# Optimization experiments

Measured on AMD Instinct MI355X. Metric: run time of the kernel, lower is better.

## Reference

```python
import jax, jax.numpy as jnp
import numpy as np

N_NODES = 100000
N_EDGES = 1600000
NUM_GRAPHS = 128
EPS = 1e-5


def setup_inputs() -> dict:
    key = jax.random.key(0)
    ks = jax.random.split(key, 8)
    x = jax.random.normal(ks[0], (N_NODES, 8), dtype=jnp.float32)
    edge_index = jax.random.randint(ks[1], (2, N_EDGES), 0, N_NODES, dtype=jnp.int64)
    batch = jnp.sort(jax.random.randint(ks[2], (N_NODES,), 0, NUM_GRAPHS, dtype=jnp.int64))
    W1_l = jax.random.normal(ks[3], (128, 8), dtype=jnp.float32) * 0.3
    b1 = jnp.zeros((128,), dtype=jnp.float32)
    W1_r = jax.random.normal(ks[4], (128, 8), dtype=jnp.float32) * 0.3
    g1 = jnp.ones((128,), dtype=jnp.float32)
    beta1 = jnp.zeros((128,), dtype=jnp.float32)
    W2_l = jax.random.normal(ks[5], (128, 128), dtype=jnp.float32) * 0.08
    b2 = jnp.zeros((128,), dtype=jnp.float32)
    W2_r = jax.random.normal(ks[6], (128, 128), dtype=jnp.float32) * 0.08
    g2 = jnp.ones((128,), dtype=jnp.float32)
    beta2 = jnp.zeros((128,), dtype=jnp.float32)
    return dict(x=x, edge_index=edge_index, batch=batch,
                W1_l=W1_l, b1=b1, W1_r=W1_r, g1=g1, beta1=beta1,
                W2_l=W2_l, b2=b2, W2_r=W2_r, g2=g2, beta2=beta2)


def _sage_conv(x, src, dst, W_l, b, W_r):
    # PyG SAGEConv: out = lin_l(mean_j x_j) + lin_r(x_i); lin_r has no bias
    msg = x[src]                                              # [E, F]
    agg = jax.ops.segment_sum(msg, dst, num_segments=N_NODES)
    deg = jax.ops.segment_sum(jnp.ones((src.shape[0],), x.dtype), dst,
                              num_segments=N_NODES)
    agg = agg / jnp.maximum(deg, 1.0)[:, None]                # mean aggregation
    return agg @ W_l.T + b + x @ W_r.T


def _batch_norm(h, gamma, beta):
    # training-mode BN over the node dimension
    mu = jnp.mean(h, axis=0)
    var = jnp.mean(jnp.square(h - mu), axis=0)
    return gamma * (h - mu) * jax.lax.rsqrt(var + EPS) + beta


def reference(x, edge_index, batch, W1_l, b1, W1_r, g1, beta1,
              W2_l, b2, W2_r, g2, beta2):
    src, dst = edge_index[0], edge_index[1]
    x1 = jax.nn.relu(_batch_norm(_sage_conv(x, src, dst, W1_l, b1, W1_r), g1, beta1))
    x2 = jax.nn.relu(_batch_norm(_sage_conv(x1, src, dst, W2_l, b2, W2_r), g2, beta2))
    h = x1 + x2  # dropout is identity in eval mode
    # global mean pool per graph
    s = jax.ops.segment_sum(h, batch, num_segments=NUM_GRAPHS)
    cnt = jax.ops.segment_sum(jnp.ones((h.shape[0],), h.dtype), batch,
                              num_segments=NUM_GRAPHS)
    return s / jnp.maximum(cnt, 1.0)[:, None]                 # [NUM_GRAPHS, 128]
```

## Files before the change

### kernel.cpp

```cpp
#include <hip/hip_runtime.h>
#include <cstdint>
#include <cstddef>

namespace {

constexpr int N_NODES = 100000;
constexpr int N_EDGES = 1600000;
constexpr int NUM_GRAPHS = 128;
constexpr int F = 128;
constexpr float BN_EPS = 1e-5f;

constexpr int W_BUCK = 512;
constexpr int NBUCK = (N_NODES + W_BUCK - 1) / W_BUCK;
constexpr int CB = 400;
constexpr int CHUNK = N_EDGES / CB;

typedef float f32x4 __attribute__((ext_vector_type(4)));
typedef float f32x2 __attribute__((ext_vector_type(2)));
typedef short s16x8 __attribute__((ext_vector_type(8)));
typedef unsigned char uchar;
union B8 { uint4 u; s16x8 s; };

__device__ inline ushort f2bf(float x) {
    uint u = __float_as_uint(x);
    u += 0x7fffu + ((u >> 16) & 1u);
    return (ushort)(u >> 16);
}
__device__ inline float bf2f(ushort s) { return __uint_as_float(((uint)s) << 16); }
__device__ inline uint pack2(float lo, float hi) {
    return (uint)f2bf(lo) | ((uint)f2bf(hi) << 16);
}
__device__ inline float bflo(uint u) { return __uint_as_float(u << 16); }
__device__ inline float bfhi(uint u) { return __uint_as_float(u & 0xffff0000u); }

__device__ inline void acc4f8(float* a, uint u) {
    f32x2 lo = __builtin_amdgcn_cvt_pk_f32_fp8((int)u, false);
    f32x2 hi = __builtin_amdgcn_cvt_pk_f32_fp8((int)u, true);
    a[0] += lo[0]; a[1] += lo[1]; a[2] += hi[0]; a[3] += hi[1];
}


__global__ void __launch_bounds__(256) k_histA(const int* __restrict__ ei,
                                               int* __restrict__ gcount) {
    __shared__ int bins[NBUCK];
    int t = threadIdx.x;
    for (int i = t; i < NBUCK; i += 256) bins[i] = 0;
    __syncthreads();
    int e0 = blockIdx.x * CHUNK;
    for (int i = t; i < CHUNK; i += 256)
        atomicAdd(&bins[ei[N_EDGES + e0 + i] >> 9], 1);
    __syncthreads();
    for (int i = t; i < NBUCK; i += 256) gcount[i * CB + blockIdx.x] = bins[i];
}

__global__ void __launch_bounds__(512) k_scanA(int* __restrict__ g,
                                               int* __restrict__ bsum) {
    __shared__ int tmp[512];
    int b = blockIdx.x, t = threadIdx.x;
    int v = (t < CB) ? g[b * CB + t] : 0;
    tmp[t] = v;
    __syncthreads();
    #pragma unroll
    for (int d = 1; d < 512; d <<= 1) {
        int u = (t >= d) ? tmp[t - d] : 0;
        __syncthreads();
        tmp[t] += u;
        __syncthreads();
    }
    if (t < CB) g[b * CB + t] = tmp[t] - v;
    if (t == 511) bsum[b] = tmp[511];
}

__global__ void __launch_bounds__(256) k_scanB(int* __restrict__ bsum) {
    __shared__ int tmp[256];
    int t = threadIdx.x;
    int v = (t < NBUCK) ? bsum[t] : 0;
    tmp[t] = v;
    __syncthreads();
    #pragma unroll
    for (int d = 1; d < 256; d <<= 1) {
        int u = (t >= d) ? tmp[t - d] : 0;
        __syncthreads();
        tmp[t] += u;
        __syncthreads();
    }
    if (t < NBUCK) bsum[t] = tmp[t] - v;
}

__global__ void __launch_bounds__(256) k_part(const int* __restrict__ ei,
                                              const int* __restrict__ gloc,
                                              const int* __restrict__ bsum,
                                              uint* __restrict__ epk) {
    __shared__ int cur[NBUCK];
    int t = threadIdx.x;
    for (int i = t; i < NBUCK; i += 256)
        cur[i] = gloc[i * CB + blockIdx.x] + bsum[i];
    __syncthreads();
    int e0 = blockIdx.x * CHUNK;
    for (int i = t; i < CHUNK; i += 256) {
        int d = ei[N_EDGES + e0 + i];
        int s = ei[e0 + i];
        int p = atomicAdd(&cur[d >> 9], 1);
        epk[p] = ((uint)s << 9) | (uint)(d & 511);
    }
}

__global__ void __launch_bounds__(512) k_rank(const uint* __restrict__ epk,
                                              const int* __restrict__ bsum,
                                              int* __restrict__ offs,
                                              int* __restrict__ ssrc) {
    __shared__ int dcnt[W_BUCK];
    __shared__ int tmp[W_BUCK];
    __shared__ int cur[W_BUCK];
    int b = blockIdx.x, t = threadIdx.x;
    dcnt[t] = 0;
    __syncthreads();
    int s0 = bsum[b];
    int s1 = (b + 1 < NBUCK) ? bsum[b + 1] : N_EDGES;
    for (int i = s0 + t; i < s1; i += 512)
        atomicAdd(&dcnt[epk[i] & 511u], 1);
    __syncthreads();
    int v = dcnt[t];
    tmp[t] = v;
    __syncthreads();
    #pragma unroll
    for (int d = 1; d < 512; d <<= 1) {
        int u = (t >= d) ? tmp[t - d] : 0;
        __syncthreads();
        tmp[t] += u;
        __syncthreads();
    }
    int start = s0 + tmp[t] - v;
    int node = b * W_BUCK + t;
    if (node <= N_NODES) offs[node] = start;
    cur[t] = start;
    __syncthreads();
    for (int i = s0 + t; i < s1; i += 512) {
        uint u = epk[i];
        int p = atomicAdd(&cur[u & 511u], 1);
        ssrc[p] = (int)(u >> 9);
    }
}


__global__ void k_bound(const int* __restrict__ batch, int* __restrict__ gstart) {
    int i = blockIdx.x * 256 + threadIdx.x;
    if (i >= N_NODES) return;
    int b = batch[i];
    if (i == 0) {
        for (int g = 0; g <= b; ++g) gstart[g] = 0;
    } else {
        int p = batch[i - 1];
        if (p != b) for (int g = p + 1; g <= b; ++g) gstart[g] = i;
    }
    if (i == N_NODES - 1) {
        for (int g = b + 1; g <= NUM_GRAPHS; ++g) gstart[g] = N_NODES;
    }
}


__global__ void k_packbf(const float* __restrict__ Wl, const float* __restrict__ Wr,
                         ushort* __restrict__ Wcat) {
    int i = blockIdx.x * 256 + threadIdx.x;
    int f = i >> 7, k = i & 127;
    Wcat[f * 256 + k]       = f2bf(Wl[i]);
    Wcat[f * 256 + 128 + k] = f2bf(Wr[i]);
}

__global__ void k_packbf1(const float* __restrict__ W1l, const float* __restrict__ W1r,
                          ushort* __restrict__ Wcat1) {
    int i = blockIdx.x * 256 + threadIdx.x;
    int f = i >> 5, k = i & 31;
    float v = (k < 8) ? W1r[f * 8 + k] : ((k < 16) ? W1l[f * 8 + (k - 8)] : 0.f);
    Wcat1[i] = f2bf(v);
}


__global__ void k_agg1(const float* __restrict__ x, const int* __restrict__ offs,
                       const int* __restrict__ ssrc, ushort* __restrict__ xa) {
    int n = blockIdx.x * 256 + threadIdx.x;
    if (n >= N_NODES) return;
    int s0 = offs[n], s1 = offs[n + 1];
    float a0=0,a1=0,a2=0,a3=0,a4=0,a5=0,a6=0,a7=0;
    int j = s0;
    for (; j + 3 < s1; j += 4) {
        int sa = ssrc[j], sb = ssrc[j+1], sc = ssrc[j+2], sd = ssrc[j+3];
        const float4* pa = (const float4*)(x + (size_t)sa * 8);
        const float4* pb = (const float4*)(x + (size_t)sb * 8);
        const float4* pc = (const float4*)(x + (size_t)sc * 8);
        const float4* pd = (const float4*)(x + (size_t)sd * 8);
        float4 va0 = pa[0], va1 = pa[1], vb0 = pb[0], vb1 = pb[1];
        float4 vc0 = pc[0], vc1 = pc[1], vd0 = pd[0], vd1 = pd[1];
        a0 += (va0.x + vb0.x) + (vc0.x + vd0.x);
        a1 += (va0.y + vb0.y) + (vc0.y + vd0.y);
        a2 += (va0.z + vb0.z) + (vc0.z + vd0.z);
        a3 += (va0.w + vb0.w) + (vc0.w + vd0.w);
        a4 += (va1.x + vb1.x) + (vc1.x + vd1.x);
        a5 += (va1.y + vb1.y) + (vc1.y + vd1.y);
        a6 += (va1.z + vb1.z) + (vc1.z + vd1.z);
        a7 += (va1.w + vb1.w) + (vc1.w + vd1.w);
    }
    for (; j < s1; ++j) {
        const float4* xp = (const float4*)(x + (size_t)ssrc[j] * 8);
        float4 b0 = xp[0], b1 = xp[1];
        a0+=b0.x; a1+=b0.y; a2+=b0.z; a3+=b0.w;
        a4+=b1.x; a5+=b1.y; a6+=b1.z; a7+=b1.w;
    }
    int dg = s1 - s0;
    float inv = 1.0f / (float)(dg > 1 ? dg : 1);
    const float4* xp = (const float4*)(x + (size_t)n * 8);
    float4 x0 = xp[0], x1v = xp[1];
    ushort* row = xa + (size_t)n * 32;
    uint4 o0 = {pack2(x0.x, x0.y), pack2(x0.z, x0.w), pack2(x1v.x, x1v.y), pack2(x1v.z, x1v.w)};
    uint4 o1 = {pack2(a0*inv, a1*inv), pack2(a2*inv, a3*inv),
                pack2(a4*inv, a5*inv), pack2(a6*inv, a7*inv)};
    uint4 z = {0u, 0u, 0u, 0u};
    *(uint4*)(row)      = o0;
    *(uint4*)(row + 8)  = o1;
    *(uint4*)(row + 16) = z;
    *(uint4*)(row + 24) = z;
}

__global__ void __launch_bounds__(256) k_lin1(
        const ushort* __restrict__ xa, const ushort* __restrict__ Wcat1,
        const float* __restrict__ b1, ushort* __restrict__ h1bf,
        float* __restrict__ stats) {
    __shared__ ushort sOut[64 * 140];
    __shared__ float sred[256];
    int tid = threadIdx.x;
    int wave = tid >> 6, lane = tid & 63;
    int quad = lane >> 4, l16 = lane & 15;
    int n0 = blockIdx.x * 64;

    int node = n0 + wave * 16 + l16;
    int cn = (node < N_NODES) ? node : N_NODES - 1;
    B8 ta;
    ta.u = *(const uint4*)(xa + (size_t)cn * 32 + quad * 8);

    #pragma unroll
    for (int nt = 0; nt < 8; ++nt) {
        int fb = nt * 16 + l16;
        B8 tb;
        tb.u = *(const uint4*)(Wcat1 + fb * 32 + quad * 8);
        f32x4 acc = {0.f, 0.f, 0.f, 0.f};
        acc = __builtin_amdgcn_mfma_f32_16x16x32_bf16(ta.s, tb.s, acc, 0, 0, 0);
        float bb = b1[fb];
        #pragma unroll
        for (int r = 0; r < 4; ++r) {
            int row = wave * 16 + quad * 4 + r;
            sOut[row * 140 + fb] = f2bf(acc[r] + bb);
        }
    }
    __syncthreads();

    #pragma unroll
    for (int p = 0; p < 4; ++p) {
        int row = p * 16 + (tid >> 4);
        int nd = n0 + row;
        if (nd < N_NODES) {
            int c0 = (tid & 15) * 8;
            uint4 v = *(const uint4*)&sOut[row * 140 + c0];
            *(uint4*)(h1bf + (size_t)nd * F + c0) = v;
        }
    }

    int f = tid & 127, half = tid >> 7;
    float s = 0.f, s2 = 0.f;
    for (int r = half * 32; r < half * 32 + 32; ++r) {
        if (n0 + r >= N_NODES) break;
        float v = bf2f(sOut[r * 140 + f]);
        s += v; s2 += v * v;
    }
    if (half) { sred[f] = s; sred[128 + f] = s2; }
    __syncthreads();
    if (!half) {
        s += sred[f]; s2 += sred[128 + f];
        atomicAdd(&stats[f], s);
        atomicAdd(&stats[F + f], s2);
    }
}

__global__ void k_bnfin(const float* __restrict__ stats, const float* __restrict__ gamma,
                        const float* __restrict__ beta, float* __restrict__ scsh) {
    int f = threadIdx.x;
    float mu  = stats[f] * (1.0f / N_NODES);
    float var = stats[F + f] * (1.0f / N_NODES) - mu * mu;
    float sc  = gamma[f] * rsqrtf(var + BN_EPS);
    scsh[f] = sc;
    scsh[F + f] = beta[f] - mu * sc;
}

__global__ void k_bnrelu(const ushort* __restrict__ h, const float* __restrict__ scsh,
                         ushort* __restrict__ x1bf, uchar* __restrict__ x1f8) {
    int i = blockIdx.x * 256 + threadIdx.x;
    int base = i * 8;
    int f = base & (F - 1);
    float4 sc0 = *(const float4*)(scsh + f);
    float4 sc1 = *(const float4*)(scsh + f + 4);
    float4 sh0 = *(const float4*)(scsh + F + f);
    float4 sh1 = *(const float4*)(scsh + F + f + 4);
    uint4 hv = *(const uint4*)(h + base);
    float v0 = fmaxf(0.f, bflo(hv.x)*sc0.x + sh0.x);
    float v1 = fmaxf(0.f, bfhi(hv.x)*sc0.y + sh0.y);
    float v2 = fmaxf(0.f, bflo(hv.y)*sc0.z + sh0.z);
    float v3 = fmaxf(0.f, bfhi(hv.y)*sc0.w + sh0.w);
    float v4 = fmaxf(0.f, bflo(hv.z)*sc1.x + sh1.x);
    float v5 = fmaxf(0.f, bfhi(hv.z)*sc1.y + sh1.y);
    float v6 = fmaxf(0.f, bflo(hv.w)*sc1.z + sh1.z);
    float v7 = fmaxf(0.f, bfhi(hv.w)*sc1.w + sh1.w);
    uint4 o = {pack2(v0,v1), pack2(v2,v3), pack2(v4,v5), pack2(v6,v7)};
    *(uint4*)(x1bf + base) = o;
    int p0 = __builtin_amdgcn_cvt_pk_fp8_f32(v0, v1, 0, false);
    p0     = __builtin_amdgcn_cvt_pk_fp8_f32(v2, v3, p0, true);
    int p1 = __builtin_amdgcn_cvt_pk_fp8_f32(v4, v5, 0, false);
    p1     = __builtin_amdgcn_cvt_pk_fp8_f32(v6, v7, p1, true);
    uint2 o8 = {(uint)p0, (uint)p1};
    *(uint2*)(x1f8 + base) = o8;
}


__global__ void __launch_bounds__(256) k_agg2(
        const uchar* __restrict__ x1f8, const int* __restrict__ offs,
        const int* __restrict__ ssrc, ushort* __restrict__ agg2bf) {
    int t = threadIdx.x;
    int n = blockIdx.x * 32 + (t >> 3);
    int c16 = (t & 7) * 16;
    int s0 = offs[n], s1 = offs[n + 1];
    float acc[16];
    #pragma unroll
    for (int i = 0; i < 16; ++i) acc[i] = 0.f;
    int j = s0;
    for (; j + 3 < s1; j += 4) {
        int sa = ssrc[j], sb = ssrc[j+1], sc = ssrc[j+2], sd = ssrc[j+3];
        uint4 va = *(const uint4*)(x1f8 + (size_t)sa * F + c16);
        uint4 vb = *(const uint4*)(x1f8 + (size_t)sb * F + c16);
        uint4 vc = *(const uint4*)(x1f8 + (size_t)sc * F + c16);
        uint4 vd = *(const uint4*)(x1f8 + (size_t)sd * F + c16);
        acc4f8(acc,      va.x); acc4f8(acc + 4,  va.y);
        acc4f8(acc + 8,  va.z); acc4f8(acc + 12, va.w);
        acc4f8(acc,      vb.x); acc4f8(acc + 4,  vb.y);
        acc4f8(acc + 8,  vb.z); acc4f8(acc + 12, vb.w);
        acc4f8(acc,      vc.x); acc4f8(acc + 4,  vc.y);
        acc4f8(acc + 8,  vc.z); acc4f8(acc + 12, vc.w);
        acc4f8(acc,      vd.x); acc4f8(acc + 4,  vd.y);
        acc4f8(acc + 8,  vd.z); acc4f8(acc + 12, vd.w);
    }
    for (; j < s1; ++j) {
        uint4 v = *(const uint4*)(x1f8 + (size_t)ssrc[j] * F + c16);
        acc4f8(acc,      v.x); acc4f8(acc + 4,  v.y);
        acc4f8(acc + 8,  v.z); acc4f8(acc + 12, v.w);
    }
    int dg = s1 - s0;
    float inv = 1.0f / (float)(dg > 1 ? dg : 1);
    uint4 o0 = {pack2(acc[0]*inv,  acc[1]*inv),  pack2(acc[2]*inv,  acc[3]*inv),
                pack2(acc[4]*inv,  acc[5]*inv),  pack2(acc[6]*inv,  acc[7]*inv)};
    uint4 o1 = {pack2(acc[8]*inv,  acc[9]*inv),  pack2(acc[10]*inv, acc[11]*inv),
                pack2(acc[12]*inv, acc[13]*inv), pack2(acc[14]*inv, acc[15]*inv)};
    ushort* dst = agg2bf + (size_t)n * F + c16;
    *(uint4*)(dst)     = o0;
    *(uint4*)(dst + 8) = o1;
}

__device__ inline int gSw(int f, int j) { return (f << 5) | ((j + f) & 31); }

__global__ void __launch_bounds__(256, 2) k_lin2(
        const ushort* __restrict__ agg2bf, const ushort* __restrict__ x1bf,
        const ushort* __restrict__ Wcat, const float* __restrict__ b2,
        ushort* __restrict__ h2bf, float* __restrict__ stats) {
    __shared__ ushort sB[2048 * 8];
    int tid = threadIdx.x;
    int wave = tid >> 6, lane = tid & 63;
    int quad = lane >> 4, l16 = lane & 15;

    int bid = blockIdx.x;
    int ng, fh;
    if (bid < 768) {
        int g = bid >> 4, i = bid & 15;
        ng = g * 8 + (i & 7);
        fh = i >> 3;
    } else {
        int idx = bid - 768;
        ng = 384 + (idx >> 1);
        fh = idx & 1;
    }
    int fbase = fh * 64;
    int wf = wave & 1, grp = wave >> 1;
    int f0 = wf * 32 + l16;
    int f1 = f0 + 16;

    #pragma unroll
    for (int it = 0; it < 8; ++it) {
        int c = it * 256 + tid;
        int f = c >> 5, j = c & 31;
        uint4 v = *(const uint4*)(Wcat + ((size_t)(fbase + f) * 32 + j) * 8);
        *(uint4*)&sB[gSw(f, j) * 8] = v;
    }
    __syncthreads();

    float bb0 = b2[fbase + f0], bb1 = b2[fbase + f1];
    float s0 = 0.f, s0q = 0.f, s1 = 0.f, s1q = 0.f;
    int n0 = ng * 256 + grp * 128;

    s16x8 aA[8], aB[8];
    auto loadTile = [&](s16x8* a, int nb) {
        int an = nb + l16;
        if (an >= N_NODES) an = N_NODES - 1;
        #pragma unroll
        for (int ks = 0; ks < 8; ++ks) {
            const ushort* src = (ks < 4) ? agg2bf : x1bf;
            B8 tm;
            tm.u = *(const uint4*)(src + (size_t)an * F + (ks & 3) * 32 + quad * 8);
            a[ks] = tm.s;
        }
    };
    auto computeTile = [&](s16x8* a, int nb) {
        f32x4 acc0 = {0,0,0,0}, acc1 = {0,0,0,0};
        #pragma unroll
        for (int ks = 0; ks < 8; ++ks) {
            int j = (ks << 2) + quad;
            B8 tb0, tb1;
            tb0.u = *(const uint4*)&sB[gSw(f0, j) * 8];
            tb1.u = *(const uint4*)&sB[gSw(f1, j) * 8];
            acc0 = __builtin_amdgcn_mfma_f32_16x16x32_bf16(a[ks], tb0.s, acc0, 0, 0, 0);
            acc1 = __builtin_amdgcn_mfma_f32_16x16x32_bf16(a[ks], tb1.s, acc1, 0, 0, 0);
        }
        #pragma unroll
        for (int r = 0; r < 4; ++r) {
            int node = nb + quad * 4 + r;
            if (node < N_NODES) {
                float v0 = acc0[r] + bb0, v1 = acc1[r] + bb1;
                h2bf[(size_t)node * F + fbase + f0] = f2bf(v0);
                h2bf[(size_t)node * F + fbase + f1] = f2bf(v1);
                s0 += v0; s0q += v0 * v0;
                s1 += v1; s1q += v1 * v1;
            }
        }
    };

    loadTile(aA, n0);
    #pragma unroll 1
    for (int p = 0; p < 4; ++p) {
        int nb = n0 + p * 32;
        loadTile(aB, nb + 16);
        computeTile(aA, nb);
        if (p < 3) loadTile(aA, nb + 32);
        computeTile(aB, nb + 16);
    }

    s0  += __shfl_xor(s0, 16);  s0  += __shfl_xor(s0, 32);
    s0q += __shfl_xor(s0q, 16); s0q += __shfl_xor(s0q, 32);
    s1  += __shfl_xor(s1, 16);  s1  += __shfl_xor(s1, 32);
    s1q += __shfl_xor(s1q, 16); s1q += __shfl_xor(s1q, 32);
    if (quad == 0) {
        atomicAdd(&stats[fbase + f0], s0);
        atomicAdd(&stats[F + fbase + f0], s0q);
        atomicAdd(&stats[fbase + f1], s1);
        atomicAdd(&stats[F + fbase + f1], s1q);
    }
}


__global__ void k_pool(const ushort* __restrict__ x1bf, const ushort* __restrict__ h2bf,
                       const float* __restrict__ scsh2, const int* __restrict__ batch,
                       float* __restrict__ outacc) {
    int f = threadIdx.x;
    int n0 = blockIdx.x * 128;
    int n1 = min(n0 + 128, N_NODES);
    float sc = scsh2[f], sh = scsh2[F + f];
    float acc = 0.f;
    int curg = batch[n0];
    for (int n = n0; n < n1; ++n) {
        int g = batch[n];
        if (g != curg) {
            atomicAdd(&outacc[curg * F + f], acc);
            acc = 0.f; curg = g;
        }
        float v1 = bf2f(x1bf[(size_t)n * F + f]);
        float v2 = fmaxf(0.f, bf2f(h2bf[(size_t)n * F + f]) * sc + sh);
        acc += v1 + v2;
    }
    atomicAdd(&outacc[curg * F + f], acc);
}

__global__ void k_out(const float* __restrict__ outacc, const int* __restrict__ gstart,
                      float* __restrict__ out) {
    int i = blockIdx.x * 256 + threadIdx.x;
    if (i >= NUM_GRAPHS * F) return;
    int g = i >> 7;
    int c = gstart[g + 1] - gstart[g];
    out[i] = outacc[i] / (float)(c > 1 ? c : 1);
}

}

extern "C" void kernel_launch(void* const* d_in, const int* in_sizes, int n_in,
                              void* d_out, int out_size, void* d_ws, size_t ws_size,
                              hipStream_t stream) {
    const float* x     = (const float*)d_in[0];
    const int*   ei    = (const int*)d_in[1];
    const int*   batch = (const int*)d_in[2];
    const float* W1l   = (const float*)d_in[3];
    const float* b1    = (const float*)d_in[4];
    const float* W1r   = (const float*)d_in[5];
    const float* g1    = (const float*)d_in[6];
    const float* be1   = (const float*)d_in[7];
    const float* W2l   = (const float*)d_in[8];
    const float* b2    = (const float*)d_in[9];
    const float* W2r   = (const float*)d_in[10];
    const float* g2    = (const float*)d_in[11];
    const float* be2   = (const float*)d_in[12];
    float* out = (float*)d_out;

    char* w = (char*)d_ws;
    size_t o = 0;
    auto alloc = [&](size_t bytes) {
        void* p = w + o;
        o += (bytes + 511) & ~(size_t)511;
        return p;
    };
    int*    offs   = (int*)alloc((size_t)(N_NODES + 1) * 4);
    int*    gcount = (int*)alloc((size_t)NBUCK * CB * 4);
    int*    bsum   = (int*)alloc((size_t)NBUCK * 4);
    int*    ssrc   = (int*)alloc((size_t)N_EDGES * 4);
    uint*   epk    = (uint*)alloc((size_t)N_EDGES * 4);
    int*    gstart = (int*)alloc((NUM_GRAPHS + 1) * 4);
    float*  stats  = (float*)alloc(512 * 4);
    float*  scsh   = (float*)alloc(512 * 4);
    ushort* Wcat   = (ushort*)alloc((size_t)F * 256 * 2);
    ushort* Wcat1  = (ushort*)alloc((size_t)F * 32 * 2);
    float*  outacc = (float*)alloc((size_t)NUM_GRAPHS * F * 4);
    ushort* xa     = (ushort*)alloc((size_t)N_NODES * 32 * 2);
    ushort* h1bf   = (ushort*)alloc((size_t)N_NODES * F * 2);
    ushort* x1bf   = (ushort*)alloc((size_t)N_NODES * F * 2);
    uchar*  x1f8   = (uchar*)alloc((size_t)N_NODES * F);
    ushort* agg2bf = (ushort*)alloc((size_t)N_NODES * F * 2);
    ushort* h2bf   = (ushort*)alloc((size_t)N_NODES * F * 2);

    hipMemsetAsync(stats,  0, 512 * 4, stream);
    hipMemsetAsync(outacc, 0, (size_t)NUM_GRAPHS * F * 4, stream);

    k_histA<<<CB, 256, 0, stream>>>(ei, gcount);
    k_scanA<<<NBUCK, 512, 0, stream>>>(gcount, bsum);
    k_scanB<<<1, 256, 0, stream>>>(bsum);
    k_part <<<CB, 256, 0, stream>>>(ei, gcount, bsum, epk);
    k_rank <<<NBUCK, 512, 0, stream>>>(epk, bsum, offs, ssrc);
    k_bound<<<(N_NODES + 255) / 256, 256, 0, stream>>>(batch, gstart);
    k_packbf <<<64, 256, 0, stream>>>(W2l, W2r, Wcat);
    k_packbf1<<<16, 256, 0, stream>>>(W1l, W1r, Wcat1);

    k_agg1  <<<(N_NODES + 255) / 256, 256, 0, stream>>>(x, offs, ssrc, xa);
    k_lin1  <<<(N_NODES + 63) / 64, 256, 0, stream>>>(xa, Wcat1, b1, h1bf, stats);
    k_bnfin <<<1, 128, 0, stream>>>(stats, g1, be1, scsh);
    k_bnrelu<<<(N_NODES * F / 8) / 256, 256, 0, stream>>>(h1bf, scsh, x1bf, x1f8);

    k_agg2  <<<N_NODES / 32, 256, 0, stream>>>(x1f8, offs, ssrc, agg2bf);
    k_lin2  <<<((N_NODES + 255) / 256) * 2, 256, 0, stream>>>(agg2bf, x1bf, Wcat, b2,
                                                              h2bf, stats + 256);
    k_bnfin <<<1, 128, 0, stream>>>(stats + 256, g2, be2, scsh + 256);

    k_pool<<<(N_NODES + 127) / 128, 128, 0, stream>>>(x1bf, h2bf, scsh + 256, batch, outacc);
    k_out <<<(NUM_GRAPHS * F + 255) / 256, 256, 0, stream>>>(outacc, gstart, out);
}
```

Before: 331.4 us.

## Merge small setup kernels, fold scans and BN finalize into consumers, bf16 gather in agg1

Removes several tiny launches: the bucket-sum scan is recomputed inside k_part and k_rank, the BN finalize kernels are folded into k_bnrelu and k_pool, and the boundary and weight-packing kernels are merged into one k_misc launch that also converts x to bf16. k_agg1 now gathers bf16 rows (16 bytes instead of 32) and both aggregation loops are unrolled by 8 for more loads in flight. k_pool uses 256 threads covering two 64-node halves. Each consumer block redundantly recomputes the scan or BN statistics, and the bf16 inputs lower layer-1 precision.

```diff
diff --git a/kernel.cpp b/kernel.cpp
--- a/kernel.cpp
+++ b/kernel.cpp
@@ -37,6 +37,12 @@
     f32x2 lo = __builtin_amdgcn_cvt_pk_f32_fp8((int)u, false);
     f32x2 hi = __builtin_amdgcn_cvt_pk_f32_fp8((int)u, true);
     a[0] += lo[0]; a[1] += lo[1]; a[2] += hi[0]; a[3] += hi[1];
+}
+__device__ inline void acc8bf(float* a, uint4 v) {
+    a[0] += bflo(v.x); a[1] += bfhi(v.x);
+    a[2] += bflo(v.y); a[3] += bfhi(v.y);
+    a[4] += bflo(v.z); a[5] += bfhi(v.z);
+    a[6] += bflo(v.w); a[7] += bfhi(v.w);
 }
 
 
@@ -71,30 +77,25 @@
     if (t == 511) bsum[b] = tmp[511];
 }
 
-__global__ void __launch_bounds__(256) k_scanB(int* __restrict__ bsum) {
-    __shared__ int tmp[256];
-    int t = threadIdx.x;
-    int v = (t < NBUCK) ? bsum[t] : 0;
-    tmp[t] = v;
-    __syncthreads();
-    #pragma unroll
-    for (int d = 1; d < 256; d <<= 1) {
-        int u = (t >= d) ? tmp[t - d] : 0;
-        __syncthreads();
-        tmp[t] += u;
-        __syncthreads();
-    }
-    if (t < NBUCK) bsum[t] = tmp[t] - v;
-}
 
 __global__ void __launch_bounds__(256) k_part(const int* __restrict__ ei,
                                               const int* __restrict__ gloc,
                                               const int* __restrict__ bsum,
                                               uint* __restrict__ epk) {
     __shared__ int cur[NBUCK];
+    __shared__ int pref[256];
     int t = threadIdx.x;
-    for (int i = t; i < NBUCK; i += 256)
-        cur[i] = gloc[i * CB + blockIdx.x] + bsum[i];
+    int v = (t < NBUCK) ? bsum[t] : 0;
+    pref[t] = v;
+    __syncthreads();
+    #pragma unroll
+    for (int d = 1; d < 256; d <<= 1) {
+        int u = (t >= d) ? pref[t - d] : 0;
+        __syncthreads();
+        pref[t] += u;
+        __syncthreads();
+    }
+    if (t < NBUCK) cur[t] = gloc[t * CB + blockIdx.x] + (pref[t] - v);
     __syncthreads();
     int e0 = blockIdx.x * CHUNK;
     for (int i = t; i < CHUNK; i += 256) {
@@ -112,11 +113,21 @@
     __shared__ int dcnt[W_BUCK];
     __shared__ int tmp[W_BUCK];
     __shared__ int cur[W_BUCK];
+    __shared__ int pref[256];
     int b = blockIdx.x, t = threadIdx.x;
+    if (t < 256) pref[t] = (t < NBUCK) ? bsum[t] : 0;
+    __syncthreads();
+    #pragma unroll
+    for (int d = 1; d < 256; d <<= 1) {
+        int u = (t < 256 && t >= d) ? pref[t - d] : 0;
+        __syncthreads();
+        if (t < 256) pref[t] += u;
+        __syncthreads();
+    }
+    int s0 = pref[b] - bsum[b];
+    int s1 = pref[b];
     dcnt[t] = 0;
     __syncthreads();
-    int s0 = bsum[b];
-    int s1 = (b + 1 < NBUCK) ? bsum[b + 1] : N_EDGES;
     for (int i = s0 + t; i < s1; i += 512)
         atomicAdd(&dcnt[epk[i] & 511u], 1);
     __syncthreads();
@@ -143,77 +154,96 @@
 }
 
 
-__global__ void k_bound(const int* __restrict__ batch, int* __restrict__ gstart) {
-    int i = blockIdx.x * 256 + threadIdx.x;
-    if (i >= N_NODES) return;
-    int b = batch[i];
-    if (i == 0) {
-        for (int g = 0; g <= b; ++g) gstart[g] = 0;
+constexpr int MB_BOUND = (N_NODES + 255) / 256;
+constexpr int MB_PB    = 64;
+constexpr int MB_PB1   = 16;
+constexpr int MB_PX    = (N_NODES + 255) / 256;
+
+__global__ void __launch_bounds__(256) k_misc(
+        const int* __restrict__ batch, int* __restrict__ gstart,
+        const float* __restrict__ W2l, const float* __restrict__ W2r,
+        ushort* __restrict__ Wcat,
+        const float* __restrict__ W1l, const float* __restrict__ W1r,
+        ushort* __restrict__ Wcat1,
+        const float* __restrict__ x, ushort* __restrict__ xbf) {
+    int bid = blockIdx.x, t = threadIdx.x;
+    if (bid < MB_BOUND) {
+        int i = bid * 256 + t;
+        if (i >= N_NODES) return;
+        int b = batch[i];
+        if (i == 0) {
+            for (int g = 0; g <= b; ++g) gstart[g] = 0;
+        } else {
+            int p = batch[i - 1];
+            if (p != b) for (int g = p + 1; g <= b; ++g) gstart[g] = i;
+        }
+        if (i == N_NODES - 1) {
+            for (int g = b + 1; g <= NUM_GRAPHS; ++g) gstart[g] = N_NODES;
+        }
+    } else if (bid < MB_BOUND + MB_PB) {
+        int i = (bid - MB_BOUND) * 256 + t;
+        int f = i >> 7, k = i & 127;
+        Wcat[f * 256 + k]       = f2bf(W2l[i]);
+        Wcat[f * 256 + 128 + k] = f2bf(W2r[i]);
+    } else if (bid < MB_BOUND + MB_PB + MB_PB1) {
+        int i = (bid - MB_BOUND - MB_PB) * 256 + t;
+        int f = i >> 5, k = i & 31;
+        float v = (k < 8) ? W1r[f * 8 + k] : ((k < 16) ? W1l[f * 8 + (k - 8)] : 0.f);
+        Wcat1[i] = f2bf(v);
     } else {
-        int p = batch[i - 1];
-        if (p != b) for (int g = p + 1; g <= b; ++g) gstart[g] = i;
-    }
-    if (i == N_NODES - 1) {
-        for (int g = b + 1; g <= NUM_GRAPHS; ++g) gstart[g] = N_NODES;
-    }
-}
-
-
-__global__ void k_packbf(const float* __restrict__ Wl, const float* __restrict__ Wr,
-                         ushort* __restrict__ Wcat) {
-    int i = blockIdx.x * 256 + threadIdx.x;
-    int f = i >> 7, k = i & 127;
-    Wcat[f * 256 + k]       = f2bf(Wl[i]);
-    Wcat[f * 256 + 128 + k] = f2bf(Wr[i]);
-}
-
-__global__ void k_packbf1(const float* __restrict__ W1l, const float* __restrict__ W1r,
-                          ushort* __restrict__ Wcat1) {
-    int i = blockIdx.x * 256 + threadIdx.x;
-    int f = i >> 5, k = i & 31;
-    float v = (k < 8) ? W1r[f * 8 + k] : ((k < 16) ? W1l[f * 8 + (k - 8)] : 0.f);
-    Wcat1[i] = f2bf(v);
-}
-
-
-__global__ void k_agg1(const float* __restrict__ x, const int* __restrict__ offs,
-                       const int* __restrict__ ssrc, ushort* __restrict__ xa) {
+        int n = (bid - MB_BOUND - MB_PB - MB_PB1) * 256 + t;
+        if (n >= N_NODES) return;
+        const float4* xp = (const float4*)(x + (size_t)n * 8);
+        float4 x0 = xp[0], x1 = xp[1];
+        uint4 o = {pack2(x0.x, x0.y), pack2(x0.z, x0.w),
+                   pack2(x1.x, x1.y), pack2(x1.z, x1.w)};
+        *(uint4*)(xbf + (size_t)n * 8) = o;
+    }
+}
+
+
+__global__ void k_agg1(const float* __restrict__ x, const ushort* __restrict__ xbf,
+                       const int* __restrict__ offs, const int* __restrict__ ssrc,
+                       ushort* __restrict__ xa) {
     int n = blockIdx.x * 256 + threadIdx.x;
     if (n >= N_NODES) return;
     int s0 = offs[n], s1 = offs[n + 1];
-    float a0=0,a1=0,a2=0,a3=0,a4=0,a5=0,a6=0,a7=0;
+    float a[8];
+    #pragma unroll
+    for (int i = 0; i < 8; ++i) a[i] = 0.f;
     int j = s0;
+    for (; j + 7 < s1; j += 8) {
+        int i0 = ssrc[j],   i1 = ssrc[j+1], i2 = ssrc[j+2], i3 = ssrc[j+3];
+        int i4 = ssrc[j+4], i5 = ssrc[j+5], i6 = ssrc[j+6], i7 = ssrc[j+7];
+        uint4 v0 = *(const uint4*)(xbf + (size_t)i0 * 8);
+        uint4 v1 = *(const uint4*)(xbf + (size_t)i1 * 8);
+        uint4 v2 = *(const uint4*)(xbf + (size_t)i2 * 8);
+        uint4 v3 = *(const uint4*)(xbf + (size_t)i3 * 8);
+        uint4 v4 = *(const uint4*)(xbf + (size_t)i4 * 8);
+        uint4 v5 = *(const uint4*)(xbf + (size_t)i5 * 8);
+        uint4 v6 = *(const uint4*)(xbf + (size_t)i6 * 8);
+        uint4 v7 = *(const uint4*)(xbf + (size_t)i7 * 8);
+        acc8bf(a, v0); acc8bf(a, v1); acc8bf(a, v2); acc8bf(a, v3);
+        acc8bf(a, v4); acc8bf(a, v5); acc8bf(a, v6); acc8bf(a, v7);
+    }
     for (; j + 3 < s1; j += 4) {
-        int sa = ssrc[j], sb = ssrc[j+1], sc = ssrc[j+2], sd = ssrc[j+3];
-        const float4* pa = (const float4*)(x + (size_t)sa * 8);
-        const float4* pb = (const float4*)(x + (size_t)sb * 8);
-        const float4* pc = (const float4*)(x + (size_t)sc * 8);
-        const float4* pd = (const float4*)(x + (size_t)sd * 8);
-        float4 va0 = pa[0], va1 = pa[1], vb0 = pb[0], vb1 = pb[1];
-        float4 vc0 = pc[0], vc1 = pc[1], vd0 = pd[0], vd1 = pd[1];
-        a0 += (va0.x + vb0.x) + (vc0.x + vd0.x);
-        a1 += (va0.y + vb0.y) + (vc0.y + vd0.y);
-        a2 += (va0.z + vb0.z) + (vc0.z + vd0.z);
-        a3 += (va0.w + vb0.w) + (vc0.w + vd0.w);
-        a4 += (va1.x + vb1.x) + (vc1.x + vd1.x);
-        a5 += (va1.y + vb1.y) + (vc1.y + vd1.y);
-        a6 += (va1.z + vb1.z) + (vc1.z + vd1.z);
-        a7 += (va1.w + vb1.w) + (vc1.w + vd1.w);
-    }
-    for (; j < s1; ++j) {
-        const float4* xp = (const float4*)(x + (size_t)ssrc[j] * 8);
-        float4 b0 = xp[0], b1 = xp[1];
-        a0+=b0.x; a1+=b0.y; a2+=b0.z; a3+=b0.w;
-        a4+=b1.x; a5+=b1.y; a6+=b1.z; a7+=b1.w;
-    }
+        int i0 = ssrc[j], i1 = ssrc[j+1], i2 = ssrc[j+2], i3 = ssrc[j+3];
+        uint4 v0 = *(const uint4*)(xbf + (size_t)i0 * 8);
+        uint4 v1 = *(const uint4*)(xbf + (size_t)i1 * 8);
+        uint4 v2 = *(const uint4*)(xbf + (size_t)i2 * 8);
+        uint4 v3 = *(const uint4*)(xbf + (size_t)i3 * 8);
+        acc8bf(a, v0); acc8bf(a, v1); acc8bf(a, v2); acc8bf(a, v3);
+    }
+    for (; j < s1; ++j)
+        acc8bf(a, *(const uint4*)(xbf + (size_t)ssrc[j] * 8));
     int dg = s1 - s0;
     float inv = 1.0f / (float)(dg > 1 ? dg : 1);
     const float4* xp = (const float4*)(x + (size_t)n * 8);
     float4 x0 = xp[0], x1v = xp[1];
     ushort* row = xa + (size_t)n * 32;
     uint4 o0 = {pack2(x0.x, x0.y), pack2(x0.z, x0.w), pack2(x1v.x, x1v.y), pack2(x1v.z, x1v.w)};
-    uint4 o1 = {pack2(a0*inv, a1*inv), pack2(a2*inv, a3*inv),
-                pack2(a4*inv, a5*inv), pack2(a6*inv, a7*inv)};
+    uint4 o1 = {pack2(a[0]*inv, a[1]*inv), pack2(a[2]*inv, a[3]*inv),
+                pack2(a[4]*inv, a[5]*inv), pack2(a[6]*inv, a[7]*inv)};
     uint4 z = {0u, 0u, 0u, 0u};
     *(uint4*)(row)      = o0;
     *(uint4*)(row + 8)  = o1;
@@ -280,34 +310,30 @@
     }
 }
 
-__global__ void k_bnfin(const float* __restrict__ stats, const float* __restrict__ gamma,
-                        const float* __restrict__ beta, float* __restrict__ scsh) {
-    int f = threadIdx.x;
-    float mu  = stats[f] * (1.0f / N_NODES);
-    float var = stats[F + f] * (1.0f / N_NODES) - mu * mu;
-    float sc  = gamma[f] * rsqrtf(var + BN_EPS);
-    scsh[f] = sc;
-    scsh[F + f] = beta[f] - mu * sc;
-}
-
-__global__ void k_bnrelu(const ushort* __restrict__ h, const float* __restrict__ scsh,
+__global__ void k_bnrelu(const ushort* __restrict__ h, const float* __restrict__ stats,
+                         const float* __restrict__ gamma, const float* __restrict__ beta,
                          ushort* __restrict__ x1bf, uchar* __restrict__ x1f8) {
     int i = blockIdx.x * 256 + threadIdx.x;
     int base = i * 8;
     int f = base & (F - 1);
-    float4 sc0 = *(const float4*)(scsh + f);
-    float4 sc1 = *(const float4*)(scsh + f + 4);
-    float4 sh0 = *(const float4*)(scsh + F + f);
-    float4 sh1 = *(const float4*)(scsh + F + f + 4);
+    float sc[8], sh[8];
+    #pragma unroll
+    for (int k = 0; k < 8; ++k) {
+        float mu  = stats[f + k] * (1.0f / N_NODES);
+        float var = stats[F + f + k] * (1.0f / N_NODES) - mu * mu;
+        float s   = gamma[f + k] * rsqrtf(var + BN_EPS);
+        sc[k] = s;
+        sh[k] = beta[f + k] - mu * s;
+    }
     uint4 hv = *(const uint4*)(h + base);
-    float v0 = fmaxf(0.f, bflo(hv.x)*sc0.x + sh0.x);
-    float v1 = fmaxf(0.f, bfhi(hv.x)*sc0.y + sh0.y);
-    float v2 = fmaxf(0.f, bflo(hv.y)*sc0.z + sh0.z);
-    float v3 = fmaxf(0.f, bfhi(hv.y)*sc0.w + sh0.w);
-    float v4 = fmaxf(0.f, bflo(hv.z)*sc1.x + sh1.x);
-    float v5 = fmaxf(0.f, bfhi(hv.z)*sc1.y + sh1.y);
-    float v6 = fmaxf(0.f, bflo(hv.w)*sc1.z + sh1.z);
-    float v7 = fmaxf(0.f, bfhi(hv.w)*sc1.w + sh1.w);
+    float v0 = fmaxf(0.f, bflo(hv.x)*sc[0] + sh[0]);
+    float v1 = fmaxf(0.f, bfhi(hv.x)*sc[1] + sh[1]);
+    float v2 = fmaxf(0.f, bflo(hv.y)*sc[2] + sh[2]);
+    float v3 = fmaxf(0.f, bfhi(hv.y)*sc[3] + sh[3]);
+    float v4 = fmaxf(0.f, bflo(hv.z)*sc[4] + sh[4]);
+    float v5 = fmaxf(0.f, bfhi(hv.z)*sc[5] + sh[5]);
+    float v6 = fmaxf(0.f, bflo(hv.w)*sc[6] + sh[6]);
+    float v7 = fmaxf(0.f, bfhi(hv.w)*sc[7] + sh[7]);
     uint4 o = {pack2(v0,v1), pack2(v2,v3), pack2(v4,v5), pack2(v6,v7)};
     *(uint4*)(x1bf + base) = o;
     int p0 = __builtin_amdgcn_cvt_pk_fp8_f32(v0, v1, 0, false);
@@ -330,25 +356,40 @@
     #pragma unroll
     for (int i = 0; i < 16; ++i) acc[i] = 0.f;
     int j = s0;
+    for (; j + 7 < s1; j += 8) {
+        int i0 = ssrc[j],   i1 = ssrc[j+1], i2 = ssrc[j+2], i3 = ssrc[j+3];
+        int i4 = ssrc[j+4], i5 = ssrc[j+5], i6 = ssrc[j+6], i7 = ssrc[j+7];
+        uint4 v0 = *(const uint4*)(x1f8 + (size_t)i0 * F + c16);
+        uint4 v1 = *(const uint4*)(x1f8 + (size_t)i1 * F + c16);
+        uint4 v2 = *(const uint4*)(x1f8 + (size_t)i2 * F + c16);
+        uint4 v3 = *(const uint4*)(x1f8 + (size_t)i3 * F + c16);
+        uint4 v4 = *(const uint4*)(x1f8 + (size_t)i4 * F + c16);
+        uint4 v5 = *(const uint4*)(x1f8 + (size_t)i5 * F + c16);
+        uint4 v6 = *(const uint4*)(x1f8 + (size_t)i6 * F + c16);
+        uint4 v7 = *(const uint4*)(x1f8 + (size_t)i7 * F + c16);
+        acc4f8(acc, v0.x); acc4f8(acc+4, v0.y); acc4f8(acc+8, v0.z); acc4f8(acc+12, v0.w);
+        acc4f8(acc, v1.x); acc4f8(acc+4, v1.y); acc4f8(acc+8, v1.z); acc4f8(acc+12, v1.w);
+        acc4f8(acc, v2.x); acc4f8(acc+4, v2.y); acc4f8(acc+8, v2.z); acc4f8(acc+12, v2.w);
+        acc4f8(acc, v3.x); acc4f8(acc+4, v3.y); acc4f8(acc+8, v3.z); acc4f8(acc+12, v3.w);
+        acc4f8(acc, v4.x); acc4f8(acc+4, v4.y); acc4f8(acc+8, v4.z); acc4f8(acc+12, v4.w);
+        acc4f8(acc, v5.x); acc4f8(acc+4, v5.y); acc4f8(acc+8, v5.z); acc4f8(acc+12, v5.w);
+        acc4f8(acc, v6.x); acc4f8(acc+4, v6.y); acc4f8(acc+8, v6.z); acc4f8(acc+12, v6.w);
+        acc4f8(acc, v7.x); acc4f8(acc+4, v7.y); acc4f8(acc+8, v7.z); acc4f8(acc+12, v7.w);
+    }
     for (; j + 3 < s1; j += 4) {
-        int sa = ssrc[j], sb = ssrc[j+1], sc = ssrc[j+2], sd = ssrc[j+3];
-        uint4 va = *(const uint4*)(x1f8 + (size_t)sa * F + c16);
-        uint4 vb = *(const uint4*)(x1f8 + (size_t)sb * F + c16);
-        uint4 vc = *(const uint4*)(x1f8 + (size_t)sc * F + c16);
-        uint4 vd = *(const uint4*)(x1f8 + (size_t)sd * F + c16);
-        acc4f8(acc,      va.x); acc4f8(acc + 4,  va.y);
-        acc4f8(acc + 8,  va.z); acc4f8(acc + 12, va.w);
-        acc4f8(acc,      vb.x); acc4f8(acc + 4,  vb.y);
-        acc4f8(acc + 8,  vb.z); acc4f8(acc + 12, vb.w);
-        acc4f8(acc,      vc.x); acc4f8(acc + 4,  vc.y);
-        acc4f8(acc + 8,  vc.z); acc4f8(acc + 12, vc.w);
-        acc4f8(acc,      vd.x); acc4f8(acc + 4,  vd.y);
-        acc4f8(acc + 8,  vd.z); acc4f8(acc + 12, vd.w);
+        int i0 = ssrc[j], i1 = ssrc[j+1], i2 = ssrc[j+2], i3 = ssrc[j+3];
+        uint4 v0 = *(const uint4*)(x1f8 + (size_t)i0 * F + c16);
+        uint4 v1 = *(const uint4*)(x1f8 + (size_t)i1 * F + c16);
+        uint4 v2 = *(const uint4*)(x1f8 + (size_t)i2 * F + c16);
+        uint4 v3 = *(const uint4*)(x1f8 + (size_t)i3 * F + c16);
+        acc4f8(acc, v0.x); acc4f8(acc+4, v0.y); acc4f8(acc+8, v0.z); acc4f8(acc+12, v0.w);
+        acc4f8(acc, v1.x); acc4f8(acc+4, v1.y); acc4f8(acc+8, v1.z); acc4f8(acc+12, v1.w);
+        acc4f8(acc, v2.x); acc4f8(acc+4, v2.y); acc4f8(acc+8, v2.z); acc4f8(acc+12, v2.w);
+        acc4f8(acc, v3.x); acc4f8(acc+4, v3.y); acc4f8(acc+8, v3.z); acc4f8(acc+12, v3.w);
     }
     for (; j < s1; ++j) {
         uint4 v = *(const uint4*)(x1f8 + (size_t)ssrc[j] * F + c16);
-        acc4f8(acc,      v.x); acc4f8(acc + 4,  v.y);
-        acc4f8(acc + 8,  v.z); acc4f8(acc + 12, v.w);
+        acc4f8(acc, v.x); acc4f8(acc+4, v.y); acc4f8(acc+8, v.z); acc4f8(acc+12, v.w);
     }
     int dg = s1 - s0;
     float inv = 1.0f / (float)(dg > 1 ? dg : 1);
@@ -461,12 +502,18 @@
 
 
 __global__ void k_pool(const ushort* __restrict__ x1bf, const ushort* __restrict__ h2bf,
-                       const float* __restrict__ scsh2, const int* __restrict__ batch,
+                       const float* __restrict__ stats2, const float* __restrict__ gamma2,
+                       const float* __restrict__ beta2, const int* __restrict__ batch,
                        float* __restrict__ outacc) {
-    int f = threadIdx.x;
-    int n0 = blockIdx.x * 128;
-    int n1 = min(n0 + 128, N_NODES);
-    float sc = scsh2[f], sh = scsh2[F + f];
+    int f = threadIdx.x & 127;
+    int half = threadIdx.x >> 7;
+    float mu  = stats2[f] * (1.0f / N_NODES);
+    float var = stats2[F + f] * (1.0f / N_NODES) - mu * mu;
+    float sc  = gamma2[f] * rsqrtf(var + BN_EPS);
+    float sh  = beta2[f] - mu * sc;
+    int n0 = blockIdx.x * 128 + half * 64;
+    if (n0 >= N_NODES) return;
+    int n1 = min(n0 + 64, N_NODES);
     float acc = 0.f;
     int curg = batch[n0];
     for (int n = n0; n < n1; ++n) {
@@ -525,10 +572,10 @@
     uint*   epk    = (uint*)alloc((size_t)N_EDGES * 4);
     int*    gstart = (int*)alloc((NUM_GRAPHS + 1) * 4);
     float*  stats  = (float*)alloc(512 * 4);
-    float*  scsh   = (float*)alloc(512 * 4);
     ushort* Wcat   = (ushort*)alloc((size_t)F * 256 * 2);
     ushort* Wcat1  = (ushort*)alloc((size_t)F * 32 * 2);
     float*  outacc = (float*)alloc((size_t)NUM_GRAPHS * F * 4);
+    ushort* xbf    = (ushort*)alloc((size_t)N_NODES * 8 * 2);
     ushort* xa     = (ushort*)alloc((size_t)N_NODES * 32 * 2);
     ushort* h1bf   = (ushort*)alloc((size_t)N_NODES * F * 2);
     ushort* x1bf   = (ushort*)alloc((size_t)N_NODES * F * 2);
@@ -539,25 +586,24 @@
     hipMemsetAsync(stats,  0, 512 * 4, stream);
     hipMemsetAsync(outacc, 0, (size_t)NUM_GRAPHS * F * 4, stream);
 
+    k_misc<<<MB_BOUND + MB_PB + MB_PB1 + MB_PX, 256, 0, stream>>>(
+        batch, gstart, W2l, W2r, Wcat, W1l, W1r, Wcat1, x, xbf);
+
     k_histA<<<CB, 256, 0, stream>>>(ei, gcount);
     k_scanA<<<NBUCK, 512, 0, stream>>>(gcount, bsum);
-    k_scanB<<<1, 256, 0, stream>>>(bsum);
     k_part <<<CB, 256, 0, stream>>>(ei, gcount, bsum, epk);
     k_rank <<<NBUCK, 512, 0, stream>>>(epk, bsum, offs, ssrc);
-    k_bound<<<(N_NODES + 255) / 256, 256, 0, stream>>>(batch, gstart);
-    k_packbf <<<64, 256, 0, stream>>>(W2l, W2r, Wcat);
-    k_packbf1<<<16, 256, 0, stream>>>(W1l, W1r, Wcat1);
-
-    k_agg1  <<<(N_NODES + 255) / 256, 256, 0, stream>>>(x, offs, ssrc, xa);
+
+    k_agg1  <<<(N_NODES + 255) / 256, 256, 0, stream>>>(x, xbf, offs, ssrc, xa);
     k_lin1  <<<(N_NODES + 63) / 64, 256, 0, stream>>>(xa, Wcat1, b1, h1bf, stats);
-    k_bnfin <<<1, 128, 0, stream>>>(stats, g1, be1, scsh);
-    k_bnrelu<<<(N_NODES * F / 8) / 256, 256, 0, stream>>>(h1bf, scsh, x1bf, x1f8);
+    k_bnrelu<<<(N_NODES * F / 8) / 256, 256, 0, stream>>>(h1bf, stats, g1, be1,
+                                                          x1bf, x1f8);
 
     k_agg2  <<<N_NODES / 32, 256, 0, stream>>>(x1f8, offs, ssrc, agg2bf);
     k_lin2  <<<((N_NODES + 255) / 256) * 2, 256, 0, stream>>>(agg2bf, x1bf, Wcat, b2,
                                                               h2bf, stats + 256);
-    k_bnfin <<<1, 128, 0, stream>>>(stats + 256, g2, be2, scsh + 256);
-
-    k_pool<<<(N_NODES + 127) / 128, 128, 0, stream>>>(x1bf, h2bf, scsh + 256, batch, outacc);
+
+    k_pool<<<(N_NODES + 127) / 128, 256, 0, stream>>>(x1bf, h2bf, stats + 256,
+                                                      g2, be2, batch, outacc);
     k_out <<<(NUM_GRAPHS * F + 255) / 256, 256, 0, stream>>>(outacc, gstart, out);
 }
```

Result: faster. 315.9 us (-4.7%).
